# Kernel tuning notes

Hardware: AMD Instinct MI355X
Metric: run time of the kernel (lower is better)

Reference implementation:

```python
import jax, jax.numpy as jnp
import numpy as np

N = 50000          # number of nodes / output rows (len(degs))
IN_C, OUT_C = 16, 16
EDGE_F = 13        # edge feature dim fed to filter net
HID = 32           # filter-net hidden width
E_NOMINAL = 800000 # target number of edges (sum of degs)


def setup_inputs() -> dict:
    rng = np.random.default_rng(0)
    # variable per-node degrees in [0, 32], adjusted so they sum exactly to E_NOMINAL
    degs = rng.integers(0, 33, size=N).astype(np.int64)
    degs[0] = max(0, degs[0] + (E_NOMINAL - int(degs.sum())))
    E = int(degs.sum())
    # segment id of each edge = destination node (equivalent to the degs-driven loop)
    idxd = np.repeat(np.arange(N, dtype=np.int32), degs)
    idxn = rng.integers(0, N, size=E).astype(np.int32)  # source node gather index

    key = jax.random.key(0)
    k1, k2, k3, k4 = jax.random.split(key, 4)
    x = jax.random.normal(k1, (N, IN_C), jnp.float32)
    edgefeats = jax.random.normal(k2, (E, EDGE_F), jnp.float32)
    # filter net: Linear(EDGE_F->HID) -> ReLU -> Linear(HID->IN_C*OUT_C)
    W1 = jax.random.normal(k3, (EDGE_F, HID), jnp.float32) / np.float32(np.sqrt(EDGE_F))
    b1 = jnp.zeros((HID,), jnp.float32)
    W2 = jax.random.normal(k4, (HID, IN_C * OUT_C), jnp.float32) / np.float32(np.sqrt(HID))
    b2 = jnp.zeros((IN_C * OUT_C,), jnp.float32)
    return {
        "x": x, "edgefeats": edgefeats,
        "W1": W1, "b1": b1, "W2": W2, "b2": b2,
        "idxn": jnp.asarray(idxn), "idxd": jnp.asarray(idxd),
        "degs": jnp.asarray(degs.astype(np.float32)),
    }


def reference(x, edgefeats, W1, b1, W2, b2, idxn, idxd, degs):
    # filter net generates a per-edge [IN_C, OUT_C] weight matrix
    h = jax.nn.relu(edgefeats @ W1 + b1)                 # [E, HID]
    w = (h @ W2 + b2).reshape(-1, IN_C, OUT_C)           # [E, IN_C, OUT_C]
    # gather source-node features and apply per-edge matvec (bmm with [E,1,IN_C])
    sel = x[idxn]                                        # [E, IN_C]
    prod = jnp.einsum('ei,eio->eo', sel, w)              # [E, OUT_C]
    # segment-mean over each node's incoming edges; degree-0 nodes -> 0
    s = jax.ops.segment_sum(prod, idxd, num_segments=N)  # [N, OUT_C]
    d = degs[:, None]
    return jnp.where(d > 0, s / jnp.maximum(d, 1.0), jnp.float32(0.0))
```

## Files before the change

kernel.cpp:

```cpp
#include <hip/hip_runtime.h>

typedef _Float16 half2v __attribute__((ext_vector_type(2)));
typedef _Float16 half4v __attribute__((ext_vector_type(4)));
typedef _Float16 half8v __attribute__((ext_vector_type(8)));
typedef float   float4v __attribute__((ext_vector_type(4)));

#define INC     16
#define OUTC    16
#define EFN     13
#define HIDC    32
#define EPB     128
#define MAXSPAN 80

union H8 { half8v v; half2v h2[4]; };

__global__ __launch_bounds__(256) void prep(
    const float* __restrict__ W2,
    const float* __restrict__ x,
    _Float16*    __restrict__ wsB,
    _Float16*    __restrict__ wsXh,
    int nh)
{
    const int b = blockIdx.x;
    if (b < 32) {
        const int i = b * 256 + threadIdx.x;
        const int j = i & 7;
        const int l = (i >> 3) & 63;
        const int t = i >> 9;
        const int q = l >> 4, n = l & 15;
        const int kk = (j < 4) ? (q * 4 + j) : (16 + q * 4 + (j & 3));
        wsB[i] = (_Float16)W2[kk * 256 + t * 16 + n];
    } else {
        const int i = (b - 32) * 256 + threadIdx.x;
        if (i * 8 < nh) {
            const float4 v0 = ((const float4*)x)[i * 2];
            const float4 v1 = ((const float4*)x)[i * 2 + 1];
            half8v h;
            h[0] = (_Float16)v0.x; h[1] = (_Float16)v0.y;
            h[2] = (_Float16)v0.z; h[3] = (_Float16)v0.w;
            h[4] = (_Float16)v1.x; h[5] = (_Float16)v1.y;
            h[6] = (_Float16)v1.z; h[7] = (_Float16)v1.w;
            *(half8v*)(wsXh + (size_t)i * 8) = h;
        }
    }
}

__global__ __launch_bounds__(64, 3) void edge_kernel(
    const _Float16* __restrict__ xh,
    const float* __restrict__ edgefeats,
    const float* __restrict__ W1,
    const float* __restrict__ b1,
    const float* __restrict__ b2,
    const int*   __restrict__ idxn,
    const int*   __restrict__ idxd,
    const float* __restrict__ degs,
    const _Float16* __restrict__ wsB,
    float*       __restrict__ out,
    float*       __restrict__ wsPfirst,
    float*       __restrict__ wsPlast,
    int*         __restrict__ wsMeta,
    int E)
{
    __shared__ float lacc[MAXSPAN * OUTC];
    __shared__ __align__(4) unsigned char su[EPB];

    const int lane = threadIdx.x;
    const int n    = lane & 15;
    const int q    = lane >> 4;

    const long b0   = (long)blockIdx.x * EPB;
    const long bEnd = (b0 + EPB < (long)E) ? (b0 + EPB) : (long)E;
    const int  d_lo = idxd[b0];
    const int  d_hi = idxd[bEnd - 1];
    const int  span = d_hi - d_lo;

    const long Em1 = (long)E - 1;
    const int  f0  = (q < 3) ? (q * 4) : 9;

    float4 efr[8];
    #pragma unroll
    for (int t = 0; t < 8; ++t) {
        long e = b0 + t * 16 + n;
        if (e > Em1) e = Em1;
        efr[t] = *(const float4*)(edgefeats + (size_t)e * EFN + f0);
    }

    int node[8];
    #pragma unroll
    for (int t = 0; t < 8; ++t) {
        long e = b0 + t * 16 + n;
        node[t] = idxn[(e <= Em1) ? e : Em1];
    }

    H8 bfr[16];
    #pragma unroll
    for (int t = 0; t < 16; ++t)
        bfr[t].v = *(const half8v*)(wsB + ((size_t)(t * 64 + lane) * 8));

    #pragma unroll
    for (int it = 0; it < MAXSPAN * OUTC / 64; ++it) lacc[lane + it * 64] = 0.0f;
    {
        const int i2 = lane * 2;
        long e0 = b0 + i2, e1 = b0 + i2 + 1;
        if (e0 > Em1) e0 = Em1;
        if (e1 > Em1) e1 = Em1;
        const unsigned u0 = (unsigned)(idxd[e0] - d_lo);
        const unsigned u1 = (unsigned)(idxd[e1] - d_lo);
        *(unsigned short*)&su[i2] = (unsigned short)(u0 | (u1 << 8));
    }

    half4v a1, a2;
    float4v c1, c2;
    #pragma unroll
    for (int jj = 0; jj < 4; ++jj) {
        const int f = q * 4 + jj;
        const bool ok = (f < EFN);
        a1[jj] = ok ? (_Float16)W1[f * HIDC + n]      : (_Float16)0.f;
        a2[jj] = ok ? (_Float16)W1[f * HIDC + 16 + n] : (_Float16)0.f;
        c1[jj] = b1[q * 4 + jj];
        c2[jj] = b1[16 + q * 4 + jj];
    }
    half8v bfragB2;
    #pragma unroll
    for (int j = 0; j < 8; ++j) {
        _Float16 val = (_Float16)0.f;
        if (q < 2) val = (_Float16)b2[(q * 8 + j) * 16 + n];
        bfragB2[j] = val;
    }

    __syncthreads();

    half8v pxa[2], pxb[2];
    pxa[0] = *(const half8v*)(xh + (size_t)node[0] * INC);
    pxb[0] = *(const half8v*)(xh + (size_t)node[0] * INC + 8);
    pxa[1] = *(const half8v*)(xh + (size_t)node[1] * INC);
    pxb[1] = *(const half8v*)(xh + (size_t)node[1] * INC + 8);
    __builtin_amdgcn_sched_barrier(0);

    #pragma unroll
    for (int t16 = 0; t16 < 8; ++t16) {
        const int cur = t16 & 1;
        const long base = b0 + (long)t16 * 16;
        const bool vM   = (base + n < (long)E);

        const half8v xA = pxa[cur];
        const half8v xB = pxb[cur];
        if (t16 + 2 < 8) {
            pxa[cur] = *(const half8v*)(xh + (size_t)node[t16 + 2] * INC);
            pxb[cur] = *(const half8v*)(xh + (size_t)node[t16 + 2] * INC + 8);
        }
        __builtin_amdgcn_sched_barrier(0);

        const unsigned u4 = *(const unsigned*)&su[t16 * 16 + q * 4];

        H8 sa, sb_;
        sa.v = xA; sb_.v = xB;
        const half2v zz = {(_Float16)0.f, (_Float16)0.f};
        half2v selh[8];
        #pragma unroll
        for (int i = 0; i < 4; ++i) {
            selh[i]     = vM ? sa.h2[i]  : zz;
            selh[4 + i] = vM ? sb_.h2[i] : zz;
        }

        half4v efB;
        if (q < 3) {
            efB[0] = (_Float16)efr[t16].x; efB[1] = (_Float16)efr[t16].y;
            efB[2] = (_Float16)efr[t16].z; efB[3] = (_Float16)efr[t16].w;
        } else {
            efB[0] = (_Float16)efr[t16].w; efB[1] = (_Float16)0.f;
            efB[2] = (_Float16)0.f;        efB[3] = (_Float16)0.f;
        }

        const float4v hf1 = __builtin_amdgcn_mfma_f32_16x16x16f16(a1, efB, c1, 0, 0, 0);
        const float4v hf2 = __builtin_amdgcn_mfma_f32_16x16x16f16(a2, efB, c2, 0, 0, 0);

        H8 hu;
        #pragma unroll
        for (int r = 0; r < 2; ++r) {
            half2v t1 = {(_Float16)fmaxf(hf1[2*r], 0.f), (_Float16)fmaxf(hf1[2*r+1], 0.f)};
            half2v t2 = {(_Float16)fmaxf(hf2[2*r], 0.f), (_Float16)fmaxf(hf2[2*r+1], 0.f)};
            hu.h2[r]     = t1;
            hu.h2[2 + r] = t2;
        }

        float4v acc = {0.f, 0.f, 0.f, 0.f};
        #pragma unroll
        for (int t = 0; t < 16; ++t) {
            _Float16 sv = (t & 1) ? selh[t >> 1][1] : selh[t >> 1][0];
            half2v sb = {sv, sv};
            H8 a;
            a.h2[0] = sb * hu.h2[0];
            a.h2[1] = sb * hu.h2[1];
            a.h2[2] = sb * hu.h2[2];
            a.h2[3] = sb * hu.h2[3];
            acc = __builtin_amdgcn_mfma_f32_16x16x32_f16(a.v, bfr[t].v, acc, 0, 0, 0);
        }
        {
            H8 a;
            #pragma unroll
            for (int j2 = 0; j2 < 4; ++j2) {
                a.h2[j2] = (q < 2) ? selh[q * 4 + j2] : zz;
            }
            acc = __builtin_amdgcn_mfma_f32_16x16x32_f16(a.v, bfragB2, acc, 0, 0, 0);
        }

        const unsigned rep = (u4 & 0xffu) * 0x01010101u;
        if (u4 == rep) {
            atomicAdd(&lacc[(u4 & 0xffu) * OUTC + n],
                      acc[0] + acc[1] + acc[2] + acc[3]);
        } else {
            #pragma unroll
            for (int r = 0; r < 4; ++r)
                atomicAdd(&lacc[((u4 >> (8 * r)) & 0xffu) * OUTC + n], acc[r]);
        }
    }

    __syncthreads();

    const bool first_starts = (b0 == 0)        || (idxd[b0 - 1] != d_lo);
    const bool last_ends    = (bEnd == (long)E) || (idxd[bEnd]   != d_hi);

    for (int i = lane; i < (span + 1) * OUTC; i += 64) {
        const int u = i >> 4;
        const int o = i & 15;
        const int v = d_lo + u;
        const float bin = lacc[u * OUTC + o];
        const bool starts = (u > 0)    || first_starts;
        const bool ends   = (u < span) || last_ends;
        if (starts && ends) {
            const float dg = degs[v];
            out[(size_t)v * OUTC + o] = (dg > 0.0f) ? bin / dg : 0.0f;
        } else if (!starts) {
            wsPfirst[(size_t)blockIdx.x * OUTC + o] = bin;
        } else {
            wsPlast[(size_t)blockIdx.x * OUTC + o] = bin;
        }
    }
    if (lane == 0) {
        wsMeta[blockIdx.x * 4 + 0] = d_hi;
        wsMeta[blockIdx.x * 4 + 1] = last_ends ? 1 : 0;
        wsMeta[blockIdx.x * 4 + 2] =
            (((span > 0) || first_starts) && !last_ends) ? 1 : 0;
    }
}

__global__ __launch_bounds__(256) void fixup_kernel(
    const float* __restrict__ degs,
    float*       __restrict__ out,
    const float* __restrict__ wsPfirst,
    const float* __restrict__ wsPlast,
    const int*   __restrict__ wsMeta,
    int N, int nblocks)
{
    const int t = blockIdx.x * 256 + threadIdx.x;

    if (t < nblocks && wsMeta[t * 4 + 2]) {
        const int v = wsMeta[t * 4 + 0];
        float tot[OUTC];
        #pragma unroll
        for (int o = 0; o < OUTC; ++o) tot[o] = wsPlast[(size_t)t * OUTC + o];
        for (int j = t + 1; j < nblocks; ++j) {
            #pragma unroll
            for (int o = 0; o < OUTC; ++o) tot[o] += wsPfirst[(size_t)j * OUTC + o];
            if (wsMeta[j * 4 + 0] != v || wsMeta[j * 4 + 1]) break;
        }
        const float dg = degs[v];
        #pragma unroll
        for (int o = 0; o < OUTC; ++o) out[(size_t)v * OUTC + o] = tot[o] / dg;
    }

    if (t < N && degs[t] == 0.0f) {
        float4* op = (float4*)(out + (size_t)t * OUTC);
        const float4 z = make_float4(0, 0, 0, 0);
        op[0] = z; op[1] = z; op[2] = z; op[3] = z;
    }
}

extern "C" void kernel_launch(void* const* d_in, const int* in_sizes, int n_in,
                              void* d_out, int out_size, void* d_ws, size_t ws_size,
                              hipStream_t stream)
{
    const float* x         = (const float*)d_in[0];
    const float* edgefeats = (const float*)d_in[1];
    const float* W1        = (const float*)d_in[2];
    const float* b1        = (const float*)d_in[3];
    const float* W2        = (const float*)d_in[4];
    const float* b2        = (const float*)d_in[5];
    const int*   idxn      = (const int*)d_in[6];
    const int*   idxd      = (const int*)d_in[7];
    const float* degs      = (const float*)d_in[8];

    const int E = in_sizes[6];
    const int N = in_sizes[8];
    const int nblocks = (E + EPB - 1) / EPB;
    const int nh = N * INC;

    _Float16* wsB  = (_Float16*)d_ws;
    _Float16* wsXh = (_Float16*)((char*)d_ws + 16384);
    size_t xh_bytes = ((size_t)nh * 2 + 255) & ~(size_t)255;
    float* wsPfirst = (float*)((char*)d_ws + 16384 + xh_bytes);
    float* wsPlast  = wsPfirst + (size_t)nblocks * OUTC;
    int*   wsMeta   = (int*)(wsPlast + (size_t)nblocks * OUTC);

    const int xhblocks = (nh / 8 + 255) / 256;
    prep<<<32 + xhblocks, 256, 0, stream>>>(W2, x, wsB, wsXh, nh);

    edge_kernel<<<nblocks, 64, 0, stream>>>(wsXh, edgefeats, W1, b1, b2,
                                            idxn, idxd, degs, wsB, (float*)d_out,
                                            wsPfirst, wsPlast, wsMeta, E);

    const int fthreads = (N > nblocks) ? N : nblocks;
    fixup_kernel<<<(fthreads + 255) / 256, 256, 0, stream>>>(
        degs, (float*)d_out, wsPfirst, wsPlast, wsMeta, N, nblocks);
}
```

Before: 184.6 us.

## Stage edge features and indices in LDS via async global_load_lds

Per-lane register preloads of edge features, source indices and segment ids are replaced by bulk asynchronous global-to-LDS copies (global_load_lds) for full blocks, with a scalar fallback for the tail block. The loop then reads features and indices from shared memory, and the packed byte-offset segment table becomes full int segment ids. The aim is coalesced streaming loads and lower register pressure, at the cost of extra LDS footprint (which may cut occupancy) and LDS read traffic inside the loop.

```diff
diff --git a/kernel.cpp b/kernel.cpp
--- a/kernel.cpp
+++ b/kernel.cpp
@@ -11,6 +11,9 @@
 #define HIDC    32
 #define EPB     128
 #define MAXSPAN 80
+
+#define GLOBAL_AS __attribute__((address_space(1)))
+#define LDS_AS    __attribute__((address_space(3)))
 
 union H8 { half8v v; half2v h2[4]; };
 
@@ -61,8 +64,10 @@
     int*         __restrict__ wsMeta,
     int E)
 {
+    __shared__ __align__(16) float sEF[EPB * EFN];
+    __shared__ __align__(16) int   sidxn[EPB];
+    __shared__ __align__(16) int   sidxd[EPB];
     __shared__ float lacc[MAXSPAN * OUTC];
-    __shared__ __align__(4) unsigned char su[EPB];
 
     const int lane = threadIdx.x;
     const int n    = lane & 15;
@@ -70,27 +75,45 @@
 
     const long b0   = (long)blockIdx.x * EPB;
     const long bEnd = (b0 + EPB < (long)E) ? (b0 + EPB) : (long)E;
-    const int  d_lo = idxd[b0];
-    const int  d_hi = idxd[bEnd - 1];
-    const int  span = d_hi - d_lo;
-
-    const long Em1 = (long)E - 1;
-    const int  f0  = (q < 3) ? (q * 4) : 9;
-
-    float4 efr[8];
-    #pragma unroll
-    for (int t = 0; t < 8; ++t) {
-        long e = b0 + t * 16 + n;
-        if (e > Em1) e = Em1;
-        efr[t] = *(const float4*)(edgefeats + (size_t)e * EFN + f0);
-    }
-
-    int node[8];
-    #pragma unroll
-    for (int t = 0; t < 8; ++t) {
-        long e = b0 + t * 16 + n;
-        node[t] = idxn[(e <= Em1) ? e : Em1];
-    }
+    const bool full = (b0 + EPB <= (long)E);
+
+    if (full) {
+        const char* efsrc = (const char*)edgefeats + (size_t)b0 * (EFN * 4);
+        #pragma unroll
+        for (int c = 0; c < 6; ++c)
+            __builtin_amdgcn_global_load_lds(
+                (const GLOBAL_AS unsigned int*)(efsrc + c * 1024 + lane * 16),
+                (LDS_AS unsigned int*)((char*)sEF + c * 1024), 16, 0, 0);
+        if (lane < 32) {
+            __builtin_amdgcn_global_load_lds(
+                (const GLOBAL_AS unsigned int*)(efsrc + 6144 + lane * 16),
+                (LDS_AS unsigned int*)((char*)sEF + 6144), 16, 0, 0);
+            __builtin_amdgcn_global_load_lds(
+                (const GLOBAL_AS unsigned int*)((const char*)(idxn + b0) + lane * 16),
+                (LDS_AS unsigned int*)sidxn, 16, 0, 0);
+            __builtin_amdgcn_global_load_lds(
+                (const GLOBAL_AS unsigned int*)((const char*)(idxd + b0) + lane * 16),
+                (LDS_AS unsigned int*)sidxd, 16, 0, 0);
+        }
+    } else {
+        const long mx = (long)E * EFN - 1;
+        for (int i = lane; i < EPB * EFN; i += 64) {
+            long gi = b0 * EFN + i;
+            if (gi > mx) gi = mx;
+            sEF[i] = edgefeats[gi];
+        }
+        const long Ec = (long)E - 1;
+        for (int i = lane; i < EPB; i += 64) {
+            long e = b0 + i;
+            if (e > Ec) e = Ec;
+            sidxn[i] = idxn[e];
+            sidxd[i] = idxd[e];
+        }
+    }
+
+    const int d_lo = idxd[b0];
+    const int d_hi = idxd[bEnd - 1];
+    const int span = d_hi - d_lo;
 
     H8 bfr[16];
     #pragma unroll
@@ -99,15 +122,6 @@
 
     #pragma unroll
     for (int it = 0; it < MAXSPAN * OUTC / 64; ++it) lacc[lane + it * 64] = 0.0f;
-    {
-        const int i2 = lane * 2;
-        long e0 = b0 + i2, e1 = b0 + i2 + 1;
-        if (e0 > Em1) e0 = Em1;
-        if (e1 > Em1) e1 = Em1;
-        const unsigned u0 = (unsigned)(idxd[e0] - d_lo);
-        const unsigned u1 = (unsigned)(idxd[e1] - d_lo);
-        *(unsigned short*)&su[i2] = (unsigned short)(u0 | (u1 << 8));
-    }
 
     half4v a1, a2;
     float4v c1, c2;
@@ -128,30 +142,41 @@
         bfragB2[j] = val;
     }
 
+    const int f0i = (q < 3) ? (q * 4) : 9;
+
     __syncthreads();
 
-    half8v pxa[2], pxb[2];
-    pxa[0] = *(const half8v*)(xh + (size_t)node[0] * INC);
-    pxb[0] = *(const half8v*)(xh + (size_t)node[0] * INC + 8);
-    pxa[1] = *(const half8v*)(xh + (size_t)node[1] * INC);
-    pxb[1] = *(const half8v*)(xh + (size_t)node[1] * INC + 8);
+    const int nd0 = sidxn[n];
+    const int nd1 = sidxn[16 + n];
+    half8v pxa0 = *(const half8v*)(xh + (size_t)nd0 * INC);
+    half8v pxb0 = *(const half8v*)(xh + (size_t)nd0 * INC + 8);
+    half8v pxa1 = *(const half8v*)(xh + (size_t)nd1 * INC);
+    half8v pxb1 = *(const half8v*)(xh + (size_t)nd1 * INC + 8);
     __builtin_amdgcn_sched_barrier(0);
 
     #pragma unroll
     for (int t16 = 0; t16 < 8; ++t16) {
-        const int cur = t16 & 1;
         const long base = b0 + (long)t16 * 16;
         const bool vM   = (base + n < (long)E);
 
-        const half8v xA = pxa[cur];
-        const half8v xB = pxb[cur];
-        if (t16 + 2 < 8) {
-            pxa[cur] = *(const half8v*)(xh + (size_t)node[t16 + 2] * INC);
-            pxb[cur] = *(const half8v*)(xh + (size_t)node[t16 + 2] * INC + 8);
+        const half8v xA = (t16 & 1) ? pxa1 : pxa0;
+        const half8v xB = (t16 & 1) ? pxb1 : pxb0;
+        if (t16 < 6) {
+            const int ndn = sidxn[(t16 + 2) * 16 + n];
+            if (t16 & 1) {
+                pxa1 = *(const half8v*)(xh + (size_t)ndn * INC);
+                pxb1 = *(const half8v*)(xh + (size_t)ndn * INC + 8);
+            } else {
+                pxa0 = *(const half8v*)(xh + (size_t)ndn * INC);
+                pxb0 = *(const half8v*)(xh + (size_t)ndn * INC + 8);
+            }
         }
         __builtin_amdgcn_sched_barrier(0);
 
-        const unsigned u4 = *(const unsigned*)&su[t16 * 16 + q * 4];
+        const int4 dd = *(const int4*)&sidxd[t16 * 16 + q * 4];
+
+        const float* efp = sEF + (size_t)(t16 * 16 + n) * EFN + f0i;
+        const float e0 = efp[0], e1 = efp[1], e2 = efp[2], e3 = efp[3];
 
         H8 sa, sb_;
         sa.v = xA; sb_.v = xB;
@@ -165,11 +190,11 @@
 
         half4v efB;
         if (q < 3) {
-            efB[0] = (_Float16)efr[t16].x; efB[1] = (_Float16)efr[t16].y;
-            efB[2] = (_Float16)efr[t16].z; efB[3] = (_Float16)efr[t16].w;
+            efB[0] = (_Float16)e0; efB[1] = (_Float16)e1;
+            efB[2] = (_Float16)e2; efB[3] = (_Float16)e3;
         } else {
-            efB[0] = (_Float16)efr[t16].w; efB[1] = (_Float16)0.f;
-            efB[2] = (_Float16)0.f;        efB[3] = (_Float16)0.f;
+            efB[0] = (_Float16)e3; efB[1] = (_Float16)0.f;
+            efB[2] = (_Float16)0.f; efB[3] = (_Float16)0.f;
         }
 
         const float4v hf1 = __builtin_amdgcn_mfma_f32_16x16x16f16(a1, efB, c1, 0, 0, 0);
@@ -205,14 +230,14 @@
             acc = __builtin_amdgcn_mfma_f32_16x16x32_f16(a.v, bfragB2, acc, 0, 0, 0);
         }
 
-        const unsigned rep = (u4 & 0xffu) * 0x01010101u;
-        if (u4 == rep) {
-            atomicAdd(&lacc[(u4 & 0xffu) * OUTC + n],
+        if (dd.x == dd.w) {
+            atomicAdd(&lacc[(dd.x - d_lo) * OUTC + n],
                       acc[0] + acc[1] + acc[2] + acc[3]);
         } else {
-            #pragma unroll
-            for (int r = 0; r < 4; ++r)
-                atomicAdd(&lacc[((u4 >> (8 * r)) & 0xffu) * OUTC + n], acc[r]);
+            atomicAdd(&lacc[(dd.x - d_lo) * OUTC + n], acc[0]);
+            atomicAdd(&lacc[(dd.y - d_lo) * OUTC + n], acc[1]);
+            atomicAdd(&lacc[(dd.z - d_lo) * OUTC + n], acc[2]);
+            atomicAdd(&lacc[(dd.w - d_lo) * OUTC + n], acc[3]);
         }
     }
 
```

After: 158.7 us. 14.0% less time.
